# Kernel tuning notes

Measured on AMD Instinct MI355X. Metric: run time of the kernel, lower is better.

## Reference

```python
import jax, jax.numpy as jnp
import numpy as np

COST_CLASS = 1.0
COST_MASK = 5.0
COST_DICE = 5.0


def _sample_points(masks, coords):
    """Bilinear grid_sample (align_corners=False, zero padding).

    masks:  [N, H, W] float
    coords: [P, 2] in [0, 1], (x, y) order as in torch grid_sample
    returns [N, P]
    """
    H, W = masks.shape[-2], masks.shape[-1]
    # torch: grid = 2*c - 1; pixel = ((grid+1)*size - 1)/2 = c*size - 0.5
    x = coords[:, 0] * W - 0.5
    y = coords[:, 1] * H - 0.5
    x0 = jnp.floor(x)
    y0 = jnp.floor(y)
    tx = (x - x0).astype(masks.dtype)
    ty = (y - y0).astype(masks.dtype)
    x0i = x0.astype(jnp.int32)
    y0i = y0.astype(jnp.int32)

    def gather(ix, iy):
        valid = ((ix >= 0) & (ix < W) & (iy >= 0) & (iy < H)).astype(masks.dtype)
        v = masks[:, jnp.clip(iy, 0, H - 1), jnp.clip(ix, 0, W - 1)]  # [N, P]
        return v * valid

    v00 = gather(x0i, y0i)
    v01 = gather(x0i + 1, y0i)
    v10 = gather(x0i, y0i + 1)
    v11 = gather(x0i + 1, y0i + 1)
    return (v00 * (1 - tx) * (1 - ty) + v01 * tx * (1 - ty)
            + v10 * (1 - tx) * ty + v11 * tx * ty)


def _cost_one(pred_mask, pred_logits, tgt_mask, labels, coords):
    # pred_mask [Q,H,W], pred_logits [Q,C], tgt_mask [T,H,W], labels [T], coords [P,2]
    probs = jax.nn.softmax(pred_logits, axis=-1)          # [Q, C]
    cost_class = -probs[:, labels]                        # [Q, T]

    pm = _sample_points(pred_mask, coords)                # [Q, P] logits
    tm = _sample_points(tgt_mask, coords)                 # [T, P] in [0,1]
    P = pm.shape[1]

    # pair-wise sigmoid BCE: BCE(x, 1) = softplus(-x), BCE(x, 0) = softplus(x)
    ce_pos = jax.nn.softplus(-pm) / P                     # [Q, P]
    ce_neg = jax.nn.softplus(pm) / P                      # [Q, P]
    cost_mask = ce_pos @ tm.T + ce_neg @ (1.0 - tm).T     # [Q, T]

    # pair-wise dice
    sig = jax.nn.sigmoid(pm)                              # [Q, P]
    numerator = 2.0 * (sig @ tm.T)                        # [Q, T]
    denominator = sig.sum(-1)[:, None] + tm.sum(-1)[None, :]
    cost_dice = 1.0 - (numerator + 1.0) / (denominator + 1.0)

    return COST_MASK * cost_mask + COST_CLASS * cost_class + COST_DICE * cost_dice


def setup_inputs() -> dict:
    key = jax.random.key(0)
    k1, k2, k3, k4, k5 = jax.random.split(key, 5)
    B, Q, C, T, H, W, P = 8, 150, 134, 32, 160, 160, 12544
    masks_queries_logits = jax.random.normal(k1, (B, Q, H, W), dtype=jnp.float32)
    class_queries_logits = jax.random.normal(k2, (B, Q, C), dtype=jnp.float32)
    # binary target masks
    mask_labels = (jax.random.uniform(k3, (B, T, H, W)) > 0.5).astype(jnp.float32)
    class_labels = jax.random.randint(k4, (B, T), 0, 133, dtype=jnp.int64)
    point_coords = jax.random.uniform(k5, (B, P, 2), dtype=jnp.float32)
    return {
        "masks_queries_logits": masks_queries_logits,
        "class_queries_logits": class_queries_logits,
        "mask_labels": mask_labels,
        "class_labels": class_labels,
        "point_coords": point_coords,
    }


def reference(masks_queries_logits, class_queries_logits, mask_labels, class_labels, point_coords):
    # Returns the per-sample cost matrices [B, Q, T] (the GPU-side work of the
    # matcher). The scipy Hungarian assignment on these matrices is CPU-bound
    # and intentionally excluded from the kernel baseline.
    cost = jax.vmap(_cost_one)(
        masks_queries_logits, class_queries_logits, mask_labels, class_labels, point_coords
    )
    return cost
```

## Files before the change

kernel.cpp:

```cpp
#include <hip/hip_runtime.h>
#include <hip/hip_bf16.h>
#include <hip/hip_fp16.h>
#include <math.h>

#define B_ 8
#define Q_ 150
#define QP_ 160
#define C_ 134
#define T_ 32
#define H_ 160
#define W_ 160
#define P_ 12544
#define HW_ (H_ * W_)
#define HW4_ (HW_ / 4)

#define SBLK 512
#define SCHUNKS 25
#define SEG_ 56
#define KSEG 224
#define KITER 7

typedef __attribute__((ext_vector_type(8))) short short8;
typedef __attribute__((ext_vector_type(4))) float floatx4;

struct Samp {
  int i00, i01, i10, i11;
  float w00, w01, w10, w11;
};

__device__ __forceinline__ Samp make_samp(float cx, float cy) {
  float x = cx * (float)W_ - 0.5f;
  float y = cy * (float)H_ - 0.5f;
  float x0f = floorf(x), y0f = floorf(y);
  float tx = x - x0f, ty = y - y0f;
  int x0 = (int)x0f, y0 = (int)y0f;
  int x1 = x0 + 1, y1 = y0 + 1;
  bool vx0 = (x0 >= 0) && (x0 < W_);
  bool vx1 = (x1 >= 0) && (x1 < W_);
  bool vy0 = (y0 >= 0) && (y0 < H_);
  bool vy1 = (y1 >= 0) && (y1 < H_);
  int cx0 = min(max(x0, 0), W_ - 1), cx1 = min(max(x1, 0), W_ - 1);
  int cy0 = min(max(y0, 0), H_ - 1), cy1 = min(max(y1, 0), H_ - 1);
  Samp s;
  s.i00 = cy0 * W_ + cx0;
  s.i01 = cy0 * W_ + cx1;
  s.i10 = cy1 * W_ + cx0;
  s.i11 = cy1 * W_ + cx1;
  float w00 = (1.f - tx) * (1.f - ty);
  float w01 = tx * (1.f - ty);
  float w10 = (1.f - tx) * ty;
  float w11 = tx * ty;
  s.w00 = (vx0 && vy0) ? w00 : 0.f;
  s.w01 = (vx1 && vy0) ? w01 : 0.f;
  s.w10 = (vx0 && vy1) ? w10 : 0.f;
  s.w11 = (vx1 && vy1) ? w11 : 0.f;
  return s;
}

__device__ __forceinline__ float waveSum(float v) {
#pragma unroll
  for (int m = 32; m >= 1; m >>= 1) v += __shfl_xor(v, m, 64);
  return v;
}
__device__ __forceinline__ float waveMax(float v) {
#pragma unroll
  for (int m = 32; m >= 1; m >>= 1) v = fmaxf(v, __shfl_xor(v, m, 64));
  return v;
}

__device__ __forceinline__ unsigned short f2bf(float x) {
  union { __hip_bfloat16 h; unsigned short u; } cv;
  cv.h = __float2bfloat16(x);
  return cv.u;
}
__device__ __forceinline__ float bf2f(unsigned short u) {
  return __uint_as_float(((unsigned int)u) << 16);
}
__device__ __forceinline__ float h2f(unsigned short u) {
  union { __half h; unsigned short u; } cv;
  cv.u = u;
  return __half2float(cv.h);
}
__device__ __forceinline__ unsigned short f2h(float x) {
  union { __half h; unsigned short u; } cv;
  cv.h = __float2half(x);
  return cv.u;
}

__launch_bounds__(256) __global__
void samp_kernel(const float* __restrict__ coords,
                 unsigned int* __restrict__ sIdx,
                 uint2* __restrict__ sW) {
  int i = blockIdx.x * 256 + threadIdx.x;
  float2 cc = ((const float2*)coords)[i];
  Samp s = make_samp(cc.x, cc.y);
  int dx = s.i01 - s.i00;
  int dy = (s.i10 != s.i00) ? 1 : 0;
  sIdx[i] = (unsigned)s.i00 | ((unsigned)dx << 15) | ((unsigned)dy << 16);
  uint2 w;
  w.x = (unsigned)f2h(s.w00) | ((unsigned)f2h(s.w01) << 16);
  w.y = (unsigned)f2h(s.w10) | ((unsigned)f2h(s.w11) << 16);
  sW[i] = w;
}

__launch_bounds__(SBLK) __global__
void sample_kernel(const float* __restrict__ masks_q,
                   const float* __restrict__ mask_labels,
                   const unsigned int* __restrict__ sIdx,
                   const uint2* __restrict__ sW,
                   unsigned short* __restrict__ pmh,
                   unsigned short* __restrict__ tmh,
                   float* __restrict__ S_sp, float* __restrict__ S_sig,
                   float* __restrict__ S_tm) {
  __shared__ unsigned short img[HW_];
  __shared__ float red[16];
  const int x = blockIdx.x;
  const int b = blockIdx.y;
  const int tid = threadIdx.x;
  const bool isPm = (x < Q_);

  const float* src = isPm ? (masks_q + ((size_t)b * Q_ + x) * HW_)
                          : (mask_labels + ((size_t)b * T_ + (x - Q_)) * HW_);
  const float4* s4 = (const float4*)src;
  for (int i = tid; i < HW4_; i += SBLK) {
    float4 v = s4[i];
    ushort4 u;
    u.x = f2bf(v.x); u.y = f2bf(v.y); u.z = f2bf(v.z); u.w = f2bf(v.w);
    *(ushort4*)&img[4 * i] = u;
  }
  __syncthreads();

  const unsigned int* sIdxB = sIdx + (size_t)b * P_;
  const uint2* sWB = sW + (size_t)b * P_;

  if (isPm) {
    unsigned short* dst = pmh + ((size_t)b * QP_ + x) * P_;
    float ssp = 0.f, ssg = 0.f;
    for (int c = 0; c < SCHUNKS; ++c) {
      int p = c * SBLK + tid;
      if (p < P_) {
        unsigned iv = sIdxB[p];
        uint2 wv = sWB[p];
        int i00 = iv & 0x7fff;
        int i01 = i00 + ((iv >> 15) & 1);
        int ir = (iv & 0x10000) ? W_ : 0;
        float pm = h2f(wv.x & 0xffff) * bf2f(img[i00]) +
                   h2f(wv.x >> 16) * bf2f(img[i01]) +
                   h2f(wv.y & 0xffff) * bf2f(img[i00 + ir]) +
                   h2f(wv.y >> 16) * bf2f(img[i01 + ir]);
        float e = __expf(-fabsf(pm));
        float sp = fmaxf(pm, 0.f) + __logf(1.f + e);
        float r = __builtin_amdgcn_rcpf(1.f + e);
        float sg = (pm >= 0.f) ? r : e * r;
        ssp += sp;
        ssg += sg;
        dst[p] = f2bf(pm);
      }
    }
    ssp = waveSum(ssp);
    ssg = waveSum(ssg);
    int w = tid >> 6;
    if ((tid & 63) == 0) {
      red[w] = ssp;
      red[8 + w] = ssg;
    }
    __syncthreads();
    if (tid == 0) {
      float a = 0.f, bb = 0.f;
#pragma unroll
      for (int i = 0; i < 8; ++i) { a += red[i]; bb += red[8 + i]; }
      S_sp[b * Q_ + x] = a;
      S_sig[b * Q_ + x] = bb;
    }
  } else {
    const int t = x - Q_;
    unsigned short* dst = tmh + ((size_t)b * T_ + t) * P_;
    float stm = 0.f;
    for (int c = 0; c < SCHUNKS; ++c) {
      int p = c * SBLK + tid;
      if (p < P_) {
        unsigned iv = sIdxB[p];
        uint2 wv = sWB[p];
        int i00 = iv & 0x7fff;
        int i01 = i00 + ((iv >> 15) & 1);
        int ir = (iv & 0x10000) ? W_ : 0;
        float v = h2f(wv.x & 0xffff) * bf2f(img[i00]) +
                  h2f(wv.x >> 16) * bf2f(img[i01]) +
                  h2f(wv.y & 0xffff) * bf2f(img[i00 + ir]) +
                  h2f(wv.y >> 16) * bf2f(img[i01 + ir]);
        stm += v;
        dst[p] = f2bf(v);
      }
    }
    stm = waveSum(stm);
    int w = tid >> 6;
    if ((tid & 63) == 0) red[w] = stm;
    __syncthreads();
    if (tid == 0) {
      float a = 0.f;
#pragma unroll
      for (int i = 0; i < 8; ++i) a += red[i];
      S_tm[b * T_ + t] = a;
    }
  }
}

__device__ __forceinline__ short8 sig_frag(short8 a) {
  short8 out;
#pragma unroll
  for (int j = 0; j < 8; ++j) {
    float x = bf2f((unsigned short)a[j]);
    float e = __expf(-fabsf(x));
    float r = __builtin_amdgcn_rcpf(1.f + e);
    float sg = (x >= 0.f) ? r : e * r;
    out[j] = (short)f2bf(sg);
  }
  return out;
}

__launch_bounds__(320) __global__
void gemm_kernel(const unsigned short* __restrict__ pmh,
                 const unsigned short* __restrict__ tmh,
                 float* __restrict__ accD) {
  const int b = blockIdx.y;
  const int seg = blockIdx.x;
  const int w = threadIdx.x >> 6;
  const int l = threadIdx.x & 63;
  const int quad = l >> 4;
  const int mrow = l & 15;

  const unsigned short* pmb = pmh + ((size_t)b * QP_ + w * 32) * P_;
  const unsigned short* tmb = tmh + (size_t)b * T_ * P_;

  floatx4 aL[2][2];
  floatx4 aS[2][2];
#pragma unroll
  for (int i = 0; i < 2; ++i)
#pragma unroll
    for (int j = 0; j < 2; ++j) {
      aL[i][j] = (floatx4){0.f, 0.f, 0.f, 0.f};
      aS[i][j] = (floatx4){0.f, 0.f, 0.f, 0.f};
    }

  const int kbase = seg * KSEG;
#pragma unroll
  for (int ki = 0; ki < KITER; ++ki) {
    const int k0 = kbase + ki * 32 + quad * 8;
    short8 a0 = *(const short8*)(pmb + (size_t)(0 * 16 + mrow) * P_ + k0);
    short8 a1 = *(const short8*)(pmb + (size_t)(1 * 16 + mrow) * P_ + k0);
    short8 b0 = *(const short8*)(tmb + (size_t)(0 * 16 + mrow) * P_ + k0);
    short8 b1 = *(const short8*)(tmb + (size_t)(1 * 16 + mrow) * P_ + k0);
    short8 s0 = sig_frag(a0);
    short8 s1 = sig_frag(a1);
    aL[0][0] = __builtin_amdgcn_mfma_f32_16x16x32_bf16(a0, b0, aL[0][0], 0, 0, 0);
    aL[0][1] = __builtin_amdgcn_mfma_f32_16x16x32_bf16(a0, b1, aL[0][1], 0, 0, 0);
    aL[1][0] = __builtin_amdgcn_mfma_f32_16x16x32_bf16(a1, b0, aL[1][0], 0, 0, 0);
    aL[1][1] = __builtin_amdgcn_mfma_f32_16x16x32_bf16(a1, b1, aL[1][1], 0, 0, 0);
    aS[0][0] = __builtin_amdgcn_mfma_f32_16x16x32_bf16(s0, b0, aS[0][0], 0, 0, 0);
    aS[0][1] = __builtin_amdgcn_mfma_f32_16x16x32_bf16(s0, b1, aS[0][1], 0, 0, 0);
    aS[1][0] = __builtin_amdgcn_mfma_f32_16x16x32_bf16(s1, b0, aS[1][0], 0, 0, 0);
    aS[1][1] = __builtin_amdgcn_mfma_f32_16x16x32_bf16(s1, b1, aS[1][1], 0, 0, 0);
  }

#pragma unroll
  for (int mtl = 0; mtl < 2; ++mtl)
#pragma unroll
    for (int nt = 0; nt < 2; ++nt)
#pragma unroll
      for (int r = 0; r < 4; ++r) {
        int q = w * 32 + mtl * 16 + quad * 4 + r;
        int t = nt * 16 + mrow;
        atomicAdd(&accD[((size_t)(0 * B_ + b) * QP_ + q) * T_ + t], aL[mtl][nt][r]);
        atomicAdd(&accD[((size_t)(1 * B_ + b) * QP_ + q) * T_ + t], aS[mtl][nt][r]);
      }
}

__launch_bounds__(64) __global__
void final_kernel(const float* __restrict__ class_q,
                  const int* __restrict__ labels,
                  const float* __restrict__ accD,
                  const float* __restrict__ S_sp,
                  const float* __restrict__ S_sig,
                  const float* __restrict__ S_tm,
                  float* __restrict__ out) {
  const int bq = blockIdx.x;
  const int b = bq / Q_;
  const int q = bq % Q_;
  const int l = threadIdx.x;
  const float* cl = class_q + (size_t)bq * C_;

  float v = -INFINITY;
  for (int c = l; c < C_; c += 64) v = fmaxf(v, cl[c]);
  float m = waveMax(v);
  float e = 0.f;
  for (int c = l; c < C_; c += 64) e += __expf(cl[c] - m);
  float den = waveSum(e);

  if (l < T_) {
    int t = l;
    int lbl = labels[b * T_ + t];
    float prob = __expf(cl[lbl] - m) / den;
    float Dlin = accD[((size_t)(0 * B_ + b) * QP_ + q) * T_ + t];
    float Dsig = accD[((size_t)(1 * B_ + b) * QP_ + q) * T_ + t];
    float cmask = (S_sp[bq] - Dlin) * (1.f / (float)P_);
    float dice = 1.f - (2.f * Dsig + 1.f) / (S_sig[bq] + S_tm[b * T_ + t] + 1.f);
    out[(size_t)bq * T_ + t] = 5.f * cmask + 5.f * dice - prob;
  }
}

extern "C" void kernel_launch(void* const* d_in, const int* in_sizes, int n_in,
                              void* d_out, int out_size, void* d_ws,
                              size_t ws_size, hipStream_t stream) {
  const float* masks_q = (const float*)d_in[0];
  const float* class_q = (const float*)d_in[1];
  const float* mask_labels = (const float*)d_in[2];
  const int* class_labels = (const int*)d_in[3];
  const float* coords = (const float*)d_in[4];
  float* out = (float*)d_out;

  float* accD = (float*)d_ws;
  float* S_sp = accD + 2 * B_ * QP_ * T_;
  float* S_sig = S_sp + B_ * Q_;
  float* S_tm = S_sig + B_ * Q_;
  uint2* sW = (uint2*)(S_tm + B_ * T_);
  unsigned int* sIdx = (unsigned int*)(sW + (size_t)B_ * P_);
  unsigned short* pmh = (unsigned short*)(sIdx + (size_t)B_ * P_);
  unsigned short* tmh = pmh + (size_t)B_ * QP_ * P_;

  hipMemsetAsync(accD, 0, (size_t)2 * B_ * QP_ * T_ * sizeof(float), stream);
  samp_kernel<<<(B_ * P_) / 256, 256, 0, stream>>>(coords, sIdx, sW);
  sample_kernel<<<dim3(Q_ + T_, B_), SBLK, 0, stream>>>(
      masks_q, mask_labels, sIdx, sW, pmh, tmh, S_sp, S_sig, S_tm);
  gemm_kernel<<<dim3(SEG_, B_), 320, 0, stream>>>(pmh, tmh, accD);
  final_kernel<<<B_ * Q_, 64, 0, stream>>>(class_q, class_labels, accD, S_sp,
                                           S_sig, S_tm, out);
}
```

Before: 260.0 us.

## Replace atomic split-K accumulation with partial buffers and a reduce kernel

The GEMM kernel no longer atomically adds into a zeroed accumulator. Each K-segment now writes its own partial result slice, and a new reduce kernel sums the 28 slices, which also removes the memset. The sampling kernel moves to 1024-thread blocks with a branch-free main loop and a separate tail. The GEMM uses half as many segments, each twice as long. This trades atomic contention for an extra launch and extra partial-buffer traffic, and halves the GEMM grid's parallelism.

```diff
diff --git a/kernel.cpp b/kernel.cpp
--- a/kernel.cpp
+++ b/kernel.cpp
@@ -14,11 +14,13 @@
 #define HW_ (H_ * W_)
 #define HW4_ (HW_ / 4)
 
-#define SBLK 512
-#define SCHUNKS 25
-#define SEG_ 56
-#define KSEG 224
-#define KITER 7
+#define SBLK 1024
+#define SFULL 12
+#define STAIL 256
+#define SEG_ 28
+#define KSEG 448
+#define KITER 14
+#define DSTRIDE (2 * B_ * QP_ * T_)
 
 typedef __attribute__((ext_vector_type(8))) short short8;
 typedef __attribute__((ext_vector_type(4))) float floatx4;
@@ -103,6 +105,17 @@
   sW[i] = w;
 }
 
+__device__ __forceinline__ float lds_sample(const unsigned short* img,
+                                            unsigned iv, uint2 wv) {
+  int i00 = iv & 0x7fff;
+  int i01 = i00 + ((iv >> 15) & 1);
+  int ir = (iv & 0x10000) ? W_ : 0;
+  return h2f(wv.x & 0xffff) * bf2f(img[i00]) +
+         h2f(wv.x >> 16) * bf2f(img[i01]) +
+         h2f(wv.y & 0xffff) * bf2f(img[i00 + ir]) +
+         h2f(wv.y >> 16) * bf2f(img[i01 + ir]);
+}
+
 __launch_bounds__(SBLK) __global__
 void sample_kernel(const float* __restrict__ masks_q,
                    const float* __restrict__ mask_labels,
@@ -113,7 +126,7 @@
                    float* __restrict__ S_sp, float* __restrict__ S_sig,
                    float* __restrict__ S_tm) {
   __shared__ unsigned short img[HW_];
-  __shared__ float red[16];
+  __shared__ float red[32];
   const int x = blockIdx.x;
   const int b = blockIdx.y;
   const int tid = threadIdx.x;
@@ -136,39 +149,41 @@
   if (isPm) {
     unsigned short* dst = pmh + ((size_t)b * QP_ + x) * P_;
     float ssp = 0.f, ssg = 0.f;
-    for (int c = 0; c < SCHUNKS; ++c) {
+#pragma unroll 2
+    for (int c = 0; c < SFULL; ++c) {
       int p = c * SBLK + tid;
-      if (p < P_) {
-        unsigned iv = sIdxB[p];
-        uint2 wv = sWB[p];
-        int i00 = iv & 0x7fff;
-        int i01 = i00 + ((iv >> 15) & 1);
-        int ir = (iv & 0x10000) ? W_ : 0;
-        float pm = h2f(wv.x & 0xffff) * bf2f(img[i00]) +
-                   h2f(wv.x >> 16) * bf2f(img[i01]) +
-                   h2f(wv.y & 0xffff) * bf2f(img[i00 + ir]) +
-                   h2f(wv.y >> 16) * bf2f(img[i01 + ir]);
-        float e = __expf(-fabsf(pm));
-        float sp = fmaxf(pm, 0.f) + __logf(1.f + e);
-        float r = __builtin_amdgcn_rcpf(1.f + e);
-        float sg = (pm >= 0.f) ? r : e * r;
-        ssp += sp;
-        ssg += sg;
-        dst[p] = f2bf(pm);
-      }
+      float pm = lds_sample(img, sIdxB[p], sWB[p]);
+      float e = __expf(-fabsf(pm));
+      float sp = fmaxf(pm, 0.f) + __logf(1.f + e);
+      float r = __builtin_amdgcn_rcpf(1.f + e);
+      float sg = (pm >= 0.f) ? r : e * r;
+      ssp += sp;
+      ssg += sg;
+      dst[p] = f2bf(pm);
+    }
+    if (tid < STAIL) {
+      int p = SFULL * SBLK + tid;
+      float pm = lds_sample(img, sIdxB[p], sWB[p]);
+      float e = __expf(-fabsf(pm));
+      float sp = fmaxf(pm, 0.f) + __logf(1.f + e);
+      float r = __builtin_amdgcn_rcpf(1.f + e);
+      float sg = (pm >= 0.f) ? r : e * r;
+      ssp += sp;
+      ssg += sg;
+      dst[p] = f2bf(pm);
     }
     ssp = waveSum(ssp);
     ssg = waveSum(ssg);
     int w = tid >> 6;
     if ((tid & 63) == 0) {
       red[w] = ssp;
-      red[8 + w] = ssg;
+      red[16 + w] = ssg;
     }
     __syncthreads();
     if (tid == 0) {
       float a = 0.f, bb = 0.f;
 #pragma unroll
-      for (int i = 0; i < 8; ++i) { a += red[i]; bb += red[8 + i]; }
+      for (int i = 0; i < 16; ++i) { a += red[i]; bb += red[16 + i]; }
       S_sp[b * Q_ + x] = a;
       S_sig[b * Q_ + x] = bb;
     }
@@ -176,21 +191,18 @@
     const int t = x - Q_;
     unsigned short* dst = tmh + ((size_t)b * T_ + t) * P_;
     float stm = 0.f;
-    for (int c = 0; c < SCHUNKS; ++c) {
+#pragma unroll 2
+    for (int c = 0; c < SFULL; ++c) {
       int p = c * SBLK + tid;
-      if (p < P_) {
-        unsigned iv = sIdxB[p];
-        uint2 wv = sWB[p];
-        int i00 = iv & 0x7fff;
-        int i01 = i00 + ((iv >> 15) & 1);
-        int ir = (iv & 0x10000) ? W_ : 0;
-        float v = h2f(wv.x & 0xffff) * bf2f(img[i00]) +
-                  h2f(wv.x >> 16) * bf2f(img[i01]) +
-                  h2f(wv.y & 0xffff) * bf2f(img[i00 + ir]) +
-                  h2f(wv.y >> 16) * bf2f(img[i01 + ir]);
-        stm += v;
-        dst[p] = f2bf(v);
-      }
+      float v = lds_sample(img, sIdxB[p], sWB[p]);
+      stm += v;
+      dst[p] = f2bf(v);
+    }
+    if (tid < STAIL) {
+      int p = SFULL * SBLK + tid;
+      float v = lds_sample(img, sIdxB[p], sWB[p]);
+      stm += v;
+      dst[p] = f2bf(v);
     }
     stm = waveSum(stm);
     int w = tid >> 6;
@@ -199,7 +211,7 @@
     if (tid == 0) {
       float a = 0.f;
 #pragma unroll
-      for (int i = 0; i < 8; ++i) a += red[i];
+      for (int i = 0; i < 16; ++i) a += red[i];
       S_tm[b * T_ + t] = a;
     }
   }
@@ -221,7 +233,7 @@
 __launch_bounds__(320) __global__
 void gemm_kernel(const unsigned short* __restrict__ pmh,
                  const unsigned short* __restrict__ tmh,
-                 float* __restrict__ accD) {
+                 float* __restrict__ accP) {
   const int b = blockIdx.y;
   const int seg = blockIdx.x;
   const int w = threadIdx.x >> 6;
@@ -243,7 +255,7 @@
     }
 
   const int kbase = seg * KSEG;
-#pragma unroll
+#pragma unroll 2
   for (int ki = 0; ki < KITER; ++ki) {
     const int k0 = kbase + ki * 32 + quad * 8;
     short8 a0 = *(const short8*)(pmb + (size_t)(0 * 16 + mrow) * P_ + k0);
@@ -262,6 +274,7 @@
     aS[1][1] = __builtin_amdgcn_mfma_f32_16x16x32_bf16(s1, b1, aS[1][1], 0, 0, 0);
   }
 
+  float* base = accP + (size_t)seg * DSTRIDE;
 #pragma unroll
   for (int mtl = 0; mtl < 2; ++mtl)
 #pragma unroll
@@ -270,9 +283,18 @@
       for (int r = 0; r < 4; ++r) {
         int q = w * 32 + mtl * 16 + quad * 4 + r;
         int t = nt * 16 + mrow;
-        atomicAdd(&accD[((size_t)(0 * B_ + b) * QP_ + q) * T_ + t], aL[mtl][nt][r]);
-        atomicAdd(&accD[((size_t)(1 * B_ + b) * QP_ + q) * T_ + t], aS[mtl][nt][r]);
+        base[((size_t)(0 * B_ + b) * QP_ + q) * T_ + t] = aL[mtl][nt][r];
+        base[((size_t)(1 * B_ + b) * QP_ + q) * T_ + t] = aS[mtl][nt][r];
       }
+}
+
+__launch_bounds__(256) __global__
+void reduce_kernel(const float* __restrict__ accP, float* __restrict__ accD) {
+  int i = blockIdx.x * 256 + threadIdx.x;
+  float s = 0.f;
+#pragma unroll
+  for (int seg = 0; seg < SEG_; ++seg) s += accP[(size_t)seg * DSTRIDE + i];
+  accD[i] = s;
 }
 
 __launch_bounds__(64) __global__
@@ -319,19 +341,20 @@
   float* out = (float*)d_out;
 
   float* accD = (float*)d_ws;
-  float* S_sp = accD + 2 * B_ * QP_ * T_;
+  float* accP = accD + DSTRIDE;
+  uint2* sW = (uint2*)(accP + (size_t)SEG_ * DSTRIDE);
+  unsigned int* sIdx = (unsigned int*)(sW + (size_t)B_ * P_);
+  float* S_sp = (float*)(sIdx + (size_t)B_ * P_);
   float* S_sig = S_sp + B_ * Q_;
   float* S_tm = S_sig + B_ * Q_;
-  uint2* sW = (uint2*)(S_tm + B_ * T_);
-  unsigned int* sIdx = (unsigned int*)(sW + (size_t)B_ * P_);
-  unsigned short* pmh = (unsigned short*)(sIdx + (size_t)B_ * P_);
+  unsigned short* pmh = (unsigned short*)(S_tm + B_ * T_);
   unsigned short* tmh = pmh + (size_t)B_ * QP_ * P_;
 
-  hipMemsetAsync(accD, 0, (size_t)2 * B_ * QP_ * T_ * sizeof(float), stream);
   samp_kernel<<<(B_ * P_) / 256, 256, 0, stream>>>(coords, sIdx, sW);
   sample_kernel<<<dim3(Q_ + T_, B_), SBLK, 0, stream>>>(
       masks_q, mask_labels, sIdx, sW, pmh, tmh, S_sp, S_sig, S_tm);
-  gemm_kernel<<<dim3(SEG_, B_), 320, 0, stream>>>(pmh, tmh, accD);
+  gemm_kernel<<<dim3(SEG_, B_), 320, 0, stream>>>(pmh, tmh, accP);
+  reduce_kernel<<<DSTRIDE / 256, 256, 0, stream>>>(accP, accD);
   final_kernel<<<B_ * Q_, 64, 0, stream>>>(class_q, class_labels, accD, S_sp,
                                            S_sig, S_tm, out);
 }
```

Result: faster. 244.7 us (-5.9%).
